# Performance work log

Hardware: AMD Instinct MI355X
Metric: run time of the kernel (lower is better)

## Reference

```python
import jax, jax.numpy as jnp
import numpy as np

C = 256
C8 = C // 8

def setup_inputs() -> dict:
    key = jax.random.key(0)
    ks = jax.random.split(key, 8)
    a = jax.random.normal(ks[0], (4, C, 64, 64), dtype=jnp.float32)
    s = 1.0 / np.sqrt(C)
    b_w = jax.random.normal(ks[1], (C8, C), dtype=jnp.float32) * s
    b_b = jnp.zeros((C8,), dtype=jnp.float32)
    c_w = jax.random.normal(ks[2], (C8, C), dtype=jnp.float32) * s
    c_b = jnp.zeros((C8,), dtype=jnp.float32)
    d_w = jax.random.normal(ks[3], (C, C), dtype=jnp.float32) * s
    d_b = jnp.zeros((C,), dtype=jnp.float32)
    alpha = jnp.zeros((1,), dtype=jnp.float32) + 0.5  # nonzero so attention path is exercised
    return {"a": a, "b_w": b_w, "b_b": b_b, "c_w": c_w, "c_b": c_b, "d_w": d_w, "d_b": d_b, "alpha": alpha}

def _conv1x1(x, w, b):
    # x: [n, c, h, w], w: [o, c] -> [n, o, h, w]
    return jnp.einsum('nchw,oc->nohw', x, w) + b[None, :, None, None]

def reference(a, b_w, b_b, c_w, c_b, d_w, d_b, alpha):
    n, chan, h, w = a.shape
    nhw = h * w
    b = _conv1x1(a, b_w, b_b).reshape(n, -1, nhw)   # [n, C/8, nhw]
    c = _conv1x1(a, c_w, c_b).reshape(n, -1, nhw)   # [n, C/8, nhw]
    k = jnp.einsum('nci,ncj->nij', b, c)            # [n, nhw, nhw]
    s = jax.nn.softmax(k, axis=-1)
    d = _conv1x1(a, d_w, d_b).reshape(n, -1, nhw)   # [n, C, nhw]
    kl = jnp.einsum('ncj,nij->nci', d, s)           # d @ s^T
    kl = kl.reshape(n, chan, h, w)
    return alpha * kl + a
```

## Files before the change

### kernel.cpp

```cpp
#include <hip/hip_runtime.h>
#include <hip/hip_bf16.h>

#define CCH 256
#define CQK 32
#define NHW 4096

typedef float f32x4 __attribute__((ext_vector_type(4)));
typedef _Float16 hv8 __attribute__((ext_vector_type(8)));
typedef _Float16 hv4 __attribute__((ext_vector_type(4)));
typedef __fp16 fv2 __attribute__((ext_vector_type(2)));

typedef __attribute__((address_space(3))) unsigned int lds_u32_t;
typedef __attribute__((address_space(1))) const unsigned int glb_u32_t;
__device__ __forceinline__ void gll16(const _Float16* gp, _Float16* lp) {
    __builtin_amdgcn_global_load_lds((glb_u32_t*)gp, (lds_u32_t*)lp, 16, 0, 0);
}

__global__ __launch_bounds__(256) void prep_kernel(
    const float* __restrict__ b_w, const float* __restrict__ c_w,
    const float* __restrict__ d_w, _Float16* __restrict__ Wh)
{
    const int bid = blockIdx.x, tid = threadIdx.x;
    const int idx = (bid * 256 + tid) * 4;
    const int row = idx >> 8, col = idx & 255;
    const float* src = (row < 32) ? (b_w + row * CCH + col)
                     : (row < 64) ? (c_w + (row - 32) * CCH + col)
                                  : (d_w + (row - 64) * CCH + col);
    const float scl = (row < 32) ? 1.4426950408889634f : 1.0f;
    float4 v = *reinterpret_cast<const float4*>(src);
    _Float16* dst = Wh + (size_t)row * CCH + col;
    dst[0] = (_Float16)(v.x * scl); dst[1] = (_Float16)(v.y * scl);
    dst[2] = (_Float16)(v.z * scl); dst[3] = (_Float16)(v.w * scl);
}

__global__ __launch_bounds__(256) void proj_kernel(
    const float* __restrict__ a, const _Float16* __restrict__ Wh,
    const float* __restrict__ b_b, const float* __restrict__ c_b,
    const float* __restrict__ d_b,
    _Float16* __restrict__ bqT, _Float16* __restrict__ ckT,
    _Float16* __restrict__ dv)
{
    __shared__ _Float16 aT[32][CCH + 24];
    __shared__ _Float16 oT[256][34];
    __shared__ _Float16 pqT[32][34];
    __shared__ _Float16 pkT[32][34];

    const int n    = blockIdx.x >> 7;
    const int i0   = (blockIdx.x & 127) << 5;
    const int tid  = threadIdx.x;
    const int lane = tid & 63;
    const int wave = tid >> 6;
    const int l15  = lane & 15;
    const int quad = lane >> 4;

    {
        const float* ap = a + (size_t)(n*CCH + tid)*NHW + i0;
        #pragma unroll
        for (int j = 0; j < 8; ++j) {
            float4 v = *reinterpret_cast<const float4*>(ap + j*4);
            aT[j*4+0][tid] = (_Float16)v.x;
            aT[j*4+1][tid] = (_Float16)v.y;
            aT[j*4+2][tid] = (_Float16)v.z;
            aT[j*4+3][tid] = (_Float16)v.w;
        }
    }
    __syncthreads();

    const f32x4 zf = {0.f, 0.f, 0.f, 0.f};
    f32x4 acc[5][2];
    #pragma unroll
    for (int t = 0; t < 5; ++t) { acc[t][0] = zf; acc[t][1] = zf; }

    const int ch0w = wave * 80;

    #pragma unroll
    for (int ks = 0; ks < 8; ++ks) {
        const int k0 = ks * 32;
        hv8 af0 = *reinterpret_cast<const hv8*>(&aT[l15][k0 + quad*8]);
        hv8 af1 = *reinterpret_cast<const hv8*>(&aT[16 + l15][k0 + quad*8]);
        #pragma unroll
        for (int t = 0; t < 5; ++t) {
            const int ch0 = ch0w + t*16;
            hv8 bf = *reinterpret_cast<const hv8*>(
                Wh + (size_t)(ch0 + l15)*CCH + k0 + quad*8);
            acc[t][0] = __builtin_amdgcn_mfma_f32_16x16x32_f16(af0, bf, acc[t][0], 0, 0, 0);
            acc[t][1] = __builtin_amdgcn_mfma_f32_16x16x32_f16(af1, bf, acc[t][1], 0, 0, 0);
        }
    }

    const int posq = quad*4;
    #pragma unroll
    for (int t = 0; t < 5; ++t) {
        const int ch0 = ch0w + t*16;
        if (ch0 < 64) {
            const float* bias_arr = (ch0 < 32) ? b_b : c_b;
            const int    ch       = (ch0 & 31) + l15;
            const float  bias     = bias_arr[ch] *
                ((ch0 < 32) ? 1.4426950408889634f : 1.0f);
            #pragma unroll
            for (int nf = 0; nf < 2; ++nf) {
                #pragma unroll
                for (int r = 0; r < 4; ++r) {
                    const int pos = posq + nf*16 + r;
                    if (ch0 < 32) pqT[pos][ch] = (_Float16)(acc[t][nf][r] + bias);
                    else          pkT[pos][ch] = (_Float16)(acc[t][nf][r] + bias);
                }
            }
        } else {
            const int ch   = ch0 - 64 + l15;
            const float bias = d_b[ch];
            #pragma unroll
            for (int nf = 0; nf < 2; ++nf) {
                hv4 v = { (_Float16)(acc[t][nf][0] + bias),
                          (_Float16)(acc[t][nf][1] + bias),
                          (_Float16)(acc[t][nf][2] + bias),
                          (_Float16)(acc[t][nf][3] + bias) };
                *reinterpret_cast<hv4*>(&oT[ch][posq + nf*16]) = v;
            }
        }
    }
    __syncthreads();

    {
        const int p   = (tid & 127) >> 2;
        const int seg = (tid & 3) << 3;
        if (tid < 128) {
            *reinterpret_cast<int4*>(
                bqT + ((size_t)n*NHW + i0 + p)*CQK + seg) =
                *reinterpret_cast<const int4*>(&pqT[p][seg]);
        } else {
            *reinterpret_cast<int4*>(
                ckT + ((size_t)n*NHW + i0 + p)*CQK + seg) =
                *reinterpret_cast<const int4*>(&pkT[p][seg]);
        }
    }
    #pragma unroll
    for (int pass = 0; pass < 4; ++pass) {
        const int row = pass*64 + (tid >> 2);
        const int seg = (tid & 3) << 3;
        *reinterpret_cast<int4*>(
            dv + ((size_t)(n*CCH + row))*NHW + i0 + seg) =
            *reinterpret_cast<const int4*>(&oT[row][seg]);
    }
}

__global__ __launch_bounds__(512, 2) void attn_kernel(
    const _Float16* __restrict__ bqT, const _Float16* __restrict__ ckT,
    const _Float16* __restrict__ dv,
    const float* __restrict__ a, const float* __restrict__ alpha_p,
    float* __restrict__ out)
{
    __shared__ __align__(16) char smem[143360];

    const int bx   = ((blockIdx.x & 7) << 5) | (blockIdx.x >> 3);
    const int n    = bx >> 6;
    const int cg   = (bx >> 5) & 1;
    const int qt   = bx & 31;
    const int q0b  = qt << 7;
    const int co0  = cg << 7;
    const int tid  = threadIdx.x;
    const int wave = tid >> 6;
    const int g    = wave >> 1;
    const int qw   = wave & 1;
    const int lane = tid & 63;
    const int l15  = lane & 15;
    const int quad = lane >> 4;
    const int kg0  = g << 10;

    _Float16* vbuf = (_Float16*)(smem + (g << 14));
    _Float16* pb   = (_Float16*)(smem + 65536 + wave*9216);
    float*    lbuf = (float*)(smem + 139264);
    float*    mbuf = (float*)(smem + 141312);

    const f32x4 zf = {0.f, 0.f, 0.f, 0.f};
    const _Float16 one_h = (_Float16)1.0f;
    const hv8 ones = { one_h, one_h, one_h, one_h, one_h, one_h, one_h, one_h };

    hv8 qf[4];
    #pragma unroll
    for (int X = 0; X < 4; ++X) {
        const int q = q0b + qw*64 + X*16 + l15;
        qf[X] = *reinterpret_cast<const hv8*>(
            bqT + ((size_t)n*NHW + q)*CQK + quad*8);
    }

    const _Float16* ckbase = ckT + ((size_t)(n*NHW + kg0 + l15))*CQK + quad*8;

    float mneg[4];
    {
        float mx[4] = {-1e30f, -1e30f, -1e30f, -1e30f};
        #pragma unroll
        for (int bt = 0; bt < 8; ++bt) {
            hv8 kb[8];
            #pragma unroll
            for (int j = 0; j < 8; ++j)
                kb[j] = *reinterpret_cast<const hv8*>(
                    ckbase + (size_t)(bt*128 + j*16)*CQK);
            #pragma unroll
            for (int X = 0; X < 4; ++X) {
                float bm[8];
                #pragma unroll
                for (int j = 0; j < 8; ++j) {
                    f32x4 s = __builtin_amdgcn_mfma_f32_16x16x32_f16(
                        kb[j], qf[X], zf, 0, 0, 0);
                    bm[j] = fmaxf(fmaxf(s[0], s[1]), fmaxf(s[2], s[3]));
                }
                float m0 = fmaxf(fmaxf(bm[0], bm[1]), fmaxf(bm[2], bm[3]));
                float m1 = fmaxf(fmaxf(bm[4], bm[5]), fmaxf(bm[6], bm[7]));
                mx[X] = fmaxf(mx[X], fmaxf(m0, m1));
            }
        }
        #pragma unroll
        for (int X = 0; X < 4; ++X) {
            mx[X] = fmaxf(mx[X], __shfl_xor(mx[X], 16, 64));
            mx[X] = fmaxf(mx[X], __shfl_xor(mx[X], 32, 64));
            mneg[X] = -mx[X];
        }
    }

    f32x4 acc[4][8];
    #pragma unroll
    for (int X = 0; X < 4; ++X)
        #pragma unroll
        for (int t = 0; t < 8; ++t) acc[X][t] = zf;
    f32x4 accL[4];
    #pragma unroll
    for (int X = 0; X < 4; ++X) accL[X] = zf;

    const int rl8 = lane >> 3;
    const _Float16* dvs = dv
        + (size_t)(n*CCH + co0 + qw*64 + rl8)*NHW + kg0 + 8*((lane & 7) ^ rl8);
    _Float16* ldsb = (_Float16*)(smem + (g << 14) + qw*8192);

    const int c0h = ((quad*16) ^ ((l15 & 7) << 4)) >> 1;
    const int c1h = ((64 + quad*16) ^ ((l15 & 7) << 4)) >> 1;

    auto softmax_tile = [&](const hv8* kf) {
        #pragma unroll
        for (int X = 0; X < 4; ++X) {
            const f32x4 minit = {mneg[X], mneg[X], mneg[X], mneg[X]};
            #pragma unroll
            for (int f = 0; f < 4; ++f) {
                f32x4 s = __builtin_amdgcn_mfma_f32_16x16x32_f16(
                    kf[f], qf[X], minit, 0, 0, 0);
                float p0 = __builtin_amdgcn_exp2f(s[0]);
                float p1 = __builtin_amdgcn_exp2f(s[1]);
                float p2 = __builtin_amdgcn_exp2f(s[2]);
                float p3 = __builtin_amdgcn_exp2f(s[3]);
                fv2 lo = __builtin_amdgcn_cvt_pkrtz(p0, p1);
                fv2 hi = __builtin_amdgcn_cvt_pkrtz(p2, p3);
                uint2 w;
                w.x = __builtin_bit_cast(unsigned, lo);
                w.y = __builtin_bit_cast(unsigned, hi);
                *reinterpret_cast<uint2*>(
                    pb + X*1152 + l15*72 + f*16 + quad*4) = w;
            }
        }
    };

    hv8 pf0[4], pf1[4];
    auto read_pf = [&]() {
        #pragma unroll
        for (int X = 0; X < 4; ++X) {
            pf0[X] = *reinterpret_cast<const hv8*>(pb + X*1152 + l15*72 + quad*8);
            pf1[X] = *reinterpret_cast<const hv8*>(pb + X*1152 + l15*72 + 32 + quad*8);
        }
    };

    auto stage = [&](int kt) {
        #pragma unroll
        for (int j = 0; j < 8; ++j)
            gll16(dvs + (size_t)(j*8)*NHW + kt*64, ldsb + (size_t)(j*8)*64);
    };

    auto load_kf = [&](int key0, hv8* kf) {
        #pragma unroll
        for (int f = 0; f < 4; ++f)
            kf[f] = *reinterpret_cast<const hv8*>(
                ckbase + (size_t)(key0 + f*16)*CQK);
    };

    {
        stage(0);
        hv8 kf0[4];
        load_kf(0, kf0);
        softmax_tile(kf0);
        read_pf();
    }
    __syncthreads();

    for (int kt = 0; kt < 16; ++kt) {
        hv8 kfn[4];
        if (kt < 15) load_kf((kt + 1)*64, kfn);

        #pragma unroll
        for (int t = 0; t < 8; ++t) {
            const _Float16* vr = vbuf + (t*16 + l15)*64;
            hv8 d0 = *reinterpret_cast<const hv8*>(vr + c0h);
            #pragma unroll
            for (int X = 0; X < 4; ++X)
                acc[X][t] = __builtin_amdgcn_mfma_f32_16x16x32_f16(
                    pf0[X], d0, acc[X][t], 0, 0, 0);
            hv8 d1 = *reinterpret_cast<const hv8*>(vr + c1h);
            #pragma unroll
            for (int X = 0; X < 4; ++X)
                acc[X][t] = __builtin_amdgcn_mfma_f32_16x16x32_f16(
                    pf1[X], d1, acc[X][t], 0, 0, 0);
        }
        #pragma unroll
        for (int X = 0; X < 4; ++X) {
            accL[X] = __builtin_amdgcn_mfma_f32_16x16x32_f16(pf0[X], ones, accL[X], 0, 0, 0);
            accL[X] = __builtin_amdgcn_mfma_f32_16x16x32_f16(pf1[X], ones, accL[X], 0, 0, 0);
        }

        if (kt < 15) {
            softmax_tile(kfn);
            __syncthreads();
            stage(kt + 1);
            read_pf();
            __syncthreads();
        }
    }

    if (lane < 16) {
        #pragma unroll
        for (int X = 0; X < 4; ++X)
            mbuf[g*128 + qw*64 + X*16 + l15] = -mneg[X];
    }
    __syncthreads();

    {
        #pragma unroll
        for (int X = 0; X < 4; ++X) {
            const int qloc = qw*64 + X*16 + quad*4;
            float4 m0 = *reinterpret_cast<float4*>(&mbuf[0*128 + qloc]);
            float4 m1 = *reinterpret_cast<float4*>(&mbuf[1*128 + qloc]);
            float4 m2 = *reinterpret_cast<float4*>(&mbuf[2*128 + qloc]);
            float4 m3 = *reinterpret_cast<float4*>(&mbuf[3*128 + qloc]);
            float4 mm;
            mm.x = fmaxf(fmaxf(m0.x, m1.x), fmaxf(m2.x, m3.x));
            mm.y = fmaxf(fmaxf(m0.y, m1.y), fmaxf(m2.y, m3.y));
            mm.z = fmaxf(fmaxf(m0.z, m1.z), fmaxf(m2.z, m3.z));
            mm.w = fmaxf(fmaxf(m0.w, m1.w), fmaxf(m2.w, m3.w));
            float4 mo = (g == 0) ? m0 : (g == 1) ? m1 : (g == 2) ? m2 : m3;
            float sc0 = __builtin_amdgcn_exp2f(mo.x - mm.x);
            float sc1 = __builtin_amdgcn_exp2f(mo.y - mm.y);
            float sc2 = __builtin_amdgcn_exp2f(mo.z - mm.z);
            float sc3 = __builtin_amdgcn_exp2f(mo.w - mm.w);
            #pragma unroll
            for (int t = 0; t < 8; ++t) {
                acc[X][t][0] *= sc0; acc[X][t][1] *= sc1;
                acc[X][t][2] *= sc2; acc[X][t][3] *= sc3;
            }
            accL[X][0] *= sc0; accL[X][1] *= sc1;
            accL[X][2] *= sc2; accL[X][3] *= sc3;
        }
    }

    float* buf1 = (float*)smem;
    float* buf2 = (float*)(smem + 67584);

    if (l15 == 0) {
        #pragma unroll
        for (int X = 0; X < 4; ++X)
            *reinterpret_cast<float4*>(&lbuf[g*128 + qw*64 + X*16 + quad*4]) =
                *reinterpret_cast<float4*>(&accL[X]);
    }
    if (g == 1 || g == 3) {
        float* b = (g == 1) ? buf1 : buf2;
        #pragma unroll
        for (int X = 0; X < 4; ++X)
            #pragma unroll
            for (int t = 0; t < 8; ++t)
                *reinterpret_cast<float4*>(
                    &b[(t*16 + l15)*132 + qw*64 + X*16 + quad*4]) =
                    *reinterpret_cast<float4*>(&acc[X][t]);
    }
    __syncthreads();
    if (g == 0 || g == 2) {
        float* b = (g == 0) ? buf1 : buf2;
        #pragma unroll
        for (int X = 0; X < 4; ++X)
            #pragma unroll
            for (int t = 0; t < 8; ++t) {
                float4 p = *reinterpret_cast<float4*>(
                    &b[(t*16 + l15)*132 + qw*64 + X*16 + quad*4]);
                acc[X][t][0] += p.x; acc[X][t][1] += p.y;
                acc[X][t][2] += p.z; acc[X][t][3] += p.w;
            }
    }
    __syncthreads();
    if (g == 2) {
        #pragma unroll
        for (int X = 0; X < 4; ++X)
            #pragma unroll
            for (int t = 0; t < 8; ++t)
                *reinterpret_cast<float4*>(
                    &buf1[(t*16 + l15)*132 + qw*64 + X*16 + quad*4]) =
                    *reinterpret_cast<float4*>(&acc[X][t]);
    }
    __syncthreads();
    if (g == 0) {
        const float alpha = alpha_p[0];
        #pragma unroll
        for (int X = 0; X < 4; ++X) {
            const int qlocX = qw*64 + X*16 + quad*4;
            #pragma unroll
            for (int t = 0; t < 8; ++t) {
                float4 p = *reinterpret_cast<float4*>(
                    &buf1[(t*16 + l15)*132 + qlocX]);
                acc[X][t][0] += p.x; acc[X][t][1] += p.y;
                acc[X][t][2] += p.z; acc[X][t][3] += p.w;
            }
            float4 l0 = *reinterpret_cast<float4*>(&lbuf[0*128 + qlocX]);
            float4 l1 = *reinterpret_cast<float4*>(&lbuf[1*128 + qlocX]);
            float4 l2 = *reinterpret_cast<float4*>(&lbuf[2*128 + qlocX]);
            float4 l3 = *reinterpret_cast<float4*>(&lbuf[3*128 + qlocX]);
            f32x4 rl;
            rl[0] = alpha / (l0.x + l1.x + l2.x + l3.x);
            rl[1] = alpha / (l0.y + l1.y + l2.y + l3.y);
            rl[2] = alpha / (l0.z + l1.z + l2.z + l3.z);
            rl[3] = alpha / (l0.w + l1.w + l2.w + l3.w);
            #pragma unroll
            for (int t = 0; t < 8; ++t) {
                const size_t off =
                    ((size_t)(n*CCH + co0 + t*16 + l15))*NHW + q0b + qlocX;
                float4 av = *reinterpret_cast<const float4*>(a + off);
                float4 o;
                o.x = acc[X][t][0]*rl[0] + av.x;
                o.y = acc[X][t][1]*rl[1] + av.y;
                o.z = acc[X][t][2]*rl[2] + av.z;
                o.w = acc[X][t][3]*rl[3] + av.w;
                *reinterpret_cast<float4*>(out + off) = o;
            }
        }
    }
}

extern "C" void kernel_launch(void* const* d_in, const int* in_sizes, int n_in,
                              void* d_out, int out_size, void* d_ws, size_t ws_size,
                              hipStream_t stream)
{
    const float* a    = (const float*)d_in[0];
    const float* b_w  = (const float*)d_in[1];
    const float* b_b  = (const float*)d_in[2];
    const float* c_w  = (const float*)d_in[3];
    const float* c_b  = (const float*)d_in[4];
    const float* d_w  = (const float*)d_in[5];
    const float* d_b  = (const float*)d_in[6];
    const float* alp  = (const float*)d_in[7];
    float* out = (float*)d_out;

    _Float16* bqT  = (_Float16*)d_ws;
    _Float16* ckT  = bqT + (size_t)4*NHW*CQK;
    _Float16* dv   = ckT + (size_t)4*NHW*CQK;
    _Float16* Wh   = dv + (size_t)4*CCH*NHW;

    prep_kernel<<<80, 256, 0, stream>>>(b_w, c_w, d_w, Wh);
    proj_kernel<<<512, 256, 0, stream>>>(a, Wh, b_b, c_b, d_b, bqT, ckT, dv);
    attn_kernel<<<256, 512, 0, stream>>>(bqT, ckT, dv, a, alp, out);
}
```

Before: 164.6 us.

## Shrink attention blocks to four waves with per-wave V staging and no block barriers

Splits the attention kernel into 512 blocks of 256 threads, each covering 64 queries instead of 128. Every wave now owns a private LDS slice for V and P and walks 32-key tiles, so the main loop synchronises with explicit waitcnt and sched_barrier instead of __syncthreads. The goals are to remove block-wide barriers from the key loop, cut LDS per block so more blocks fit per CU, and fill the GPU with more blocks. In exchange each block reads the K and V tiles for only half as many queries, which roughly doubles global and L2 traffic for K/V, and the shorter MFMA chains per tile leave less latency hiding.

```diff
diff --git a/kernel.cpp b/kernel.cpp
--- a/kernel.cpp
+++ b/kernel.cpp
@@ -144,33 +144,31 @@
     }
 }
 
-__global__ __launch_bounds__(512, 2) void attn_kernel(
+__global__ __launch_bounds__(256, 2) void attn_kernel(
     const _Float16* __restrict__ bqT, const _Float16* __restrict__ ckT,
     const _Float16* __restrict__ dv,
     const float* __restrict__ a, const float* __restrict__ alpha_p,
     float* __restrict__ out)
 {
-    __shared__ __align__(16) char smem[143360];
-
-    const int bx   = ((blockIdx.x & 7) << 5) | (blockIdx.x >> 3);
-    const int n    = bx >> 6;
-    const int cg   = (bx >> 5) & 1;
-    const int qt   = bx & 31;
-    const int q0b  = qt << 7;
+    __shared__ __align__(16) char smem[72704];
+
+    const int bx   = ((blockIdx.x & 7) << 6) | (blockIdx.x >> 3);
+    const int n    = bx >> 7;
+    const int cg   = (bx >> 6) & 1;
+    const int qt   = bx & 63;
+    const int q0b  = qt << 6;
     const int co0  = cg << 7;
     const int tid  = threadIdx.x;
-    const int wave = tid >> 6;
-    const int g    = wave >> 1;
-    const int qw   = wave & 1;
+    const int g    = tid >> 6;
     const int lane = tid & 63;
     const int l15  = lane & 15;
     const int quad = lane >> 4;
     const int kg0  = g << 10;
 
-    _Float16* vbuf = (_Float16*)(smem + (g << 14));
-    _Float16* pb   = (_Float16*)(smem + 65536 + wave*9216);
-    float*    lbuf = (float*)(smem + 139264);
-    float*    mbuf = (float*)(smem + 141312);
+    _Float16* vbuf = (_Float16*)(smem + g*8192);
+    _Float16* pb   = (_Float16*)(smem + 32768 + g*5120);
+    float*    lbuf = (float*)(smem + 70656);
+    float*    mbuf = (float*)(smem + 71680);
 
     const f32x4 zf = {0.f, 0.f, 0.f, 0.f};
     const _Float16 one_h = (_Float16)1.0f;
@@ -179,7 +177,7 @@
     hv8 qf[4];
     #pragma unroll
     for (int X = 0; X < 4; ++X) {
-        const int q = q0b + qw*64 + X*16 + l15;
+        const int q = q0b + X*16 + l15;
         qf[X] = *reinterpret_cast<const hv8*>(
             bqT + ((size_t)n*NHW + q)*CQK + quad*8);
     }
@@ -227,20 +225,19 @@
     #pragma unroll
     for (int X = 0; X < 4; ++X) accL[X] = zf;
 
-    const int rl8 = lane >> 3;
+    const int rl4 = lane >> 2;
+    const int sl  = lane & 3;
     const _Float16* dvs = dv
-        + (size_t)(n*CCH + co0 + qw*64 + rl8)*NHW + kg0 + 8*((lane & 7) ^ rl8);
-    _Float16* ldsb = (_Float16*)(smem + (g << 14) + qw*8192);
-
-    const int c0h = ((quad*16) ^ ((l15 & 7) << 4)) >> 1;
-    const int c1h = ((64 + quad*16) ^ ((l15 & 7) << 4)) >> 1;
+        + (size_t)(n*CCH + co0 + rl4)*NHW + kg0 + 8*(sl ^ ((rl4 >> 1) & 3));
+
+    const int c0h = (quad*8) ^ (((l15 >> 1) & 3) << 3);
 
     auto softmax_tile = [&](const hv8* kf) {
         #pragma unroll
         for (int X = 0; X < 4; ++X) {
             const f32x4 minit = {mneg[X], mneg[X], mneg[X], mneg[X]};
             #pragma unroll
-            for (int f = 0; f < 4; ++f) {
+            for (int f = 0; f < 2; ++f) {
                 f32x4 s = __builtin_amdgcn_mfma_f32_16x16x32_f16(
                     kf[f], qf[X], minit, 0, 0, 0);
                 float p0 = __builtin_amdgcn_exp2f(s[0]);
@@ -253,90 +250,83 @@
                 w.x = __builtin_bit_cast(unsigned, lo);
                 w.y = __builtin_bit_cast(unsigned, hi);
                 *reinterpret_cast<uint2*>(
-                    pb + X*1152 + l15*72 + f*16 + quad*4) = w;
+                    pb + X*640 + l15*40 + f*16 + quad*4) = w;
             }
         }
     };
 
-    hv8 pf0[4], pf1[4];
+    hv8 pf0[4];
     auto read_pf = [&]() {
         #pragma unroll
-        for (int X = 0; X < 4; ++X) {
-            pf0[X] = *reinterpret_cast<const hv8*>(pb + X*1152 + l15*72 + quad*8);
-            pf1[X] = *reinterpret_cast<const hv8*>(pb + X*1152 + l15*72 + 32 + quad*8);
-        }
+        for (int X = 0; X < 4; ++X)
+            pf0[X] = *reinterpret_cast<const hv8*>(pb + X*640 + l15*40 + quad*8);
     };
 
     auto stage = [&](int kt) {
         #pragma unroll
         for (int j = 0; j < 8; ++j)
-            gll16(dvs + (size_t)(j*8)*NHW + kt*64, ldsb + (size_t)(j*8)*64);
+            gll16(dvs + (size_t)(j*16)*NHW + kt*32, vbuf + j*512);
     };
 
     auto load_kf = [&](int key0, hv8* kf) {
         #pragma unroll
-        for (int f = 0; f < 4; ++f)
+        for (int f = 0; f < 2; ++f)
             kf[f] = *reinterpret_cast<const hv8*>(
                 ckbase + (size_t)(key0 + f*16)*CQK);
     };
 
     {
         stage(0);
-        hv8 kf0[4];
+        hv8 kf0[2];
         load_kf(0, kf0);
         softmax_tile(kf0);
         read_pf();
-    }
-    __syncthreads();
-
-    for (int kt = 0; kt < 16; ++kt) {
-        hv8 kfn[4];
-        if (kt < 15) load_kf((kt + 1)*64, kfn);
+        asm volatile("s_waitcnt vmcnt(0)" ::: "memory");
+        __builtin_amdgcn_sched_barrier(0);
+    }
+
+    for (int kt = 0; kt < 32; ++kt) {
+        hv8 kfn[2];
+        if (kt < 31) load_kf((kt + 1)*32, kfn);
 
         #pragma unroll
         for (int t = 0; t < 8; ++t) {
-            const _Float16* vr = vbuf + (t*16 + l15)*64;
-            hv8 d0 = *reinterpret_cast<const hv8*>(vr + c0h);
+            hv8 d0 = *reinterpret_cast<const hv8*>(vbuf + (t*16 + l15)*32 + c0h);
             #pragma unroll
             for (int X = 0; X < 4; ++X)
                 acc[X][t] = __builtin_amdgcn_mfma_f32_16x16x32_f16(
                     pf0[X], d0, acc[X][t], 0, 0, 0);
-            hv8 d1 = *reinterpret_cast<const hv8*>(vr + c1h);
-            #pragma unroll
-            for (int X = 0; X < 4; ++X)
-                acc[X][t] = __builtin_amdgcn_mfma_f32_16x16x32_f16(
-                    pf1[X], d1, acc[X][t], 0, 0, 0);
-        }
+        }
+        #pragma unroll
+        for (int X = 0; X < 4; ++X)
+            accL[X] = __builtin_amdgcn_mfma_f32_16x16x32_f16(pf0[X], ones, accL[X], 0, 0, 0);
+
+        if (kt < 31) {
+            asm volatile("s_waitcnt lgkmcnt(0)" ::: "memory");
+            __builtin_amdgcn_sched_barrier(0);
+            stage(kt + 1);
+            softmax_tile(kfn);
+            read_pf();
+            asm volatile("s_waitcnt vmcnt(0)" ::: "memory");
+            __builtin_amdgcn_sched_barrier(0);
+        }
+    }
+
+    if (lane < 16) {
+        #pragma unroll
+        for (int X = 0; X < 4; ++X)
+            mbuf[g*64 + X*16 + l15] = -mneg[X];
+    }
+    __syncthreads();
+
+    {
         #pragma unroll
         for (int X = 0; X < 4; ++X) {
-            accL[X] = __builtin_amdgcn_mfma_f32_16x16x32_f16(pf0[X], ones, accL[X], 0, 0, 0);
-            accL[X] = __builtin_amdgcn_mfma_f32_16x16x32_f16(pf1[X], ones, accL[X], 0, 0, 0);
-        }
-
-        if (kt < 15) {
-            softmax_tile(kfn);
-            __syncthreads();
-            stage(kt + 1);
-            read_pf();
-            __syncthreads();
-        }
-    }
-
-    if (lane < 16) {
-        #pragma unroll
-        for (int X = 0; X < 4; ++X)
-            mbuf[g*128 + qw*64 + X*16 + l15] = -mneg[X];
-    }
-    __syncthreads();
-
-    {
-        #pragma unroll
-        for (int X = 0; X < 4; ++X) {
-            const int qloc = qw*64 + X*16 + quad*4;
-            float4 m0 = *reinterpret_cast<float4*>(&mbuf[0*128 + qloc]);
-            float4 m1 = *reinterpret_cast<float4*>(&mbuf[1*128 + qloc]);
-            float4 m2 = *reinterpret_cast<float4*>(&mbuf[2*128 + qloc]);
-            float4 m3 = *reinterpret_cast<float4*>(&mbuf[3*128 + qloc]);
+            const int qloc = X*16 + quad*4;
+            float4 m0 = *reinterpret_cast<float4*>(&mbuf[0*64 + qloc]);
+            float4 m1 = *reinterpret_cast<float4*>(&mbuf[1*64 + qloc]);
+            float4 m2 = *reinterpret_cast<float4*>(&mbuf[2*64 + qloc]);
+            float4 m3 = *reinterpret_cast<float4*>(&mbuf[3*64 + qloc]);
             float4 mm;
             mm.x = fmaxf(fmaxf(m0.x, m1.x), fmaxf(m2.x, m3.x));
             mm.y = fmaxf(fmaxf(m0.y, m1.y), fmaxf(m2.y, m3.y));
@@ -356,16 +346,24 @@
             accL[X][2] *= sc2; accL[X][3] *= sc3;
         }
     }
+    if (lane < 16) {
+        if (l15 == 0) {
+            #pragma unroll
+            for (int X = 0; X < 4; ++X)
+                *reinterpret_cast<float4*>(&lbuf[g*64 + X*16 + quad*4]) =
+                    *reinterpret_cast<float4*>(&accL[X]);
+        }
+    } else if (l15 == 0) {
+        #pragma unroll
+        for (int X = 0; X < 4; ++X)
+            *reinterpret_cast<float4*>(&lbuf[g*64 + X*16 + quad*4]) =
+                *reinterpret_cast<float4*>(&accL[X]);
+    }
+    __syncthreads();
 
     float* buf1 = (float*)smem;
-    float* buf2 = (float*)(smem + 67584);
-
-    if (l15 == 0) {
-        #pragma unroll
-        for (int X = 0; X < 4; ++X)
-            *reinterpret_cast<float4*>(&lbuf[g*128 + qw*64 + X*16 + quad*4]) =
-                *reinterpret_cast<float4*>(&accL[X]);
-    }
+    float* buf2 = (float*)(smem + 35840);
+
     if (g == 1 || g == 3) {
         float* b = (g == 1) ? buf1 : buf2;
         #pragma unroll
@@ -373,7 +371,7 @@
             #pragma unroll
             for (int t = 0; t < 8; ++t)
                 *reinterpret_cast<float4*>(
-                    &b[(t*16 + l15)*132 + qw*64 + X*16 + quad*4]) =
+                    &b[(t*16 + l15)*68 + X*16 + quad*4]) =
                     *reinterpret_cast<float4*>(&acc[X][t]);
     }
     __syncthreads();
@@ -384,7 +382,7 @@
             #pragma unroll
             for (int t = 0; t < 8; ++t) {
                 float4 p = *reinterpret_cast<float4*>(
-                    &b[(t*16 + l15)*132 + qw*64 + X*16 + quad*4]);
+                    &b[(t*16 + l15)*68 + X*16 + quad*4]);
                 acc[X][t][0] += p.x; acc[X][t][1] += p.y;
                 acc[X][t][2] += p.z; acc[X][t][3] += p.w;
             }
@@ -396,7 +394,7 @@
             #pragma unroll
             for (int t = 0; t < 8; ++t)
                 *reinterpret_cast<float4*>(
-                    &buf1[(t*16 + l15)*132 + qw*64 + X*16 + quad*4]) =
+                    &buf1[(t*16 + l15)*68 + X*16 + quad*4]) =
                     *reinterpret_cast<float4*>(&acc[X][t]);
     }
     __syncthreads();
@@ -404,18 +402,18 @@
         const float alpha = alpha_p[0];
         #pragma unroll
         for (int X = 0; X < 4; ++X) {
-            const int qlocX = qw*64 + X*16 + quad*4;
+            const int qloc = X*16 + quad*4;
             #pragma unroll
             for (int t = 0; t < 8; ++t) {
                 float4 p = *reinterpret_cast<float4*>(
-                    &buf1[(t*16 + l15)*132 + qlocX]);
+                    &buf1[(t*16 + l15)*68 + qloc]);
                 acc[X][t][0] += p.x; acc[X][t][1] += p.y;
                 acc[X][t][2] += p.z; acc[X][t][3] += p.w;
             }
-            float4 l0 = *reinterpret_cast<float4*>(&lbuf[0*128 + qlocX]);
-            float4 l1 = *reinterpret_cast<float4*>(&lbuf[1*128 + qlocX]);
-            float4 l2 = *reinterpret_cast<float4*>(&lbuf[2*128 + qlocX]);
-            float4 l3 = *reinterpret_cast<float4*>(&lbuf[3*128 + qlocX]);
+            float4 l0 = *reinterpret_cast<float4*>(&lbuf[0*64 + qloc]);
+            float4 l1 = *reinterpret_cast<float4*>(&lbuf[1*64 + qloc]);
+            float4 l2 = *reinterpret_cast<float4*>(&lbuf[2*64 + qloc]);
+            float4 l3 = *reinterpret_cast<float4*>(&lbuf[3*64 + qloc]);
             f32x4 rl;
             rl[0] = alpha / (l0.x + l1.x + l2.x + l3.x);
             rl[1] = alpha / (l0.y + l1.y + l2.y + l3.y);
@@ -424,7 +422,7 @@
             #pragma unroll
             for (int t = 0; t < 8; ++t) {
                 const size_t off =
-                    ((size_t)(n*CCH + co0 + t*16 + l15))*NHW + q0b + qlocX;
+                    ((size_t)(n*CCH + co0 + t*16 + l15))*NHW + q0b + qloc;
                 float4 av = *reinterpret_cast<const float4*>(a + off);
                 float4 o;
                 o.x = acc[X][t][0]*rl[0] + av.x;
@@ -458,5 +456,5 @@
 
     prep_kernel<<<80, 256, 0, stream>>>(b_w, c_w, d_w, Wh);
     proj_kernel<<<512, 256, 0, stream>>>(a, Wh, b_b, c_b, d_b, bqT, ckT, dv);
-    attn_kernel<<<256, 512, 0, stream>>>(bqT, ckT, dv, a, alp, out);
+    attn_kernel<<<512, 256, 0, stream>>>(bqT, ckT, dv, a, alp, out);
 }
```

After: 160.8 us. 2.3% less time.
